# Kernel tuning notes

Measured on AMD Instinct MI355X. Metric: run time of the kernel, lower is better.

Reference implementation:

```python
import jax, jax.numpy as jnp
import numpy as np

TEMPERATURE = 0.1
NUM_CLASSES = 4  # matches fill_max of labels
NEG_INF = -1e9
EPS = 1e-6


def setup_inputs() -> dict:
    key = jax.random.key(0)
    k1, k2 = jax.random.split(key)
    emb = jax.random.normal(k1, (2, 128, 64, 64), dtype=jnp.float32)
    labels = jax.random.randint(k2, (2, 64, 64), 0, NUM_CLASSES, dtype=jnp.int32)
    return {"emb": emb, "labels": labels}


def reference(emb, labels):
    B, C, H, W = emb.shape
    e = emb.transpose(0, 2, 3, 1).reshape(B * H * W, C)      # [N, C]
    lab = labels.reshape(B * H * W)                           # [N]
    # F.normalize(dim=1) with eps clamp
    norm = jnp.maximum(jnp.linalg.norm(e, axis=1, keepdims=True), 1e-12)
    e = e / norm
    n = e.shape[0]
    logits = (e @ e.T) / TEMPERATURE                          # [N, N]
    diag = jnp.arange(n)
    logits = logits.at[diag, diag].set(NEG_INF)               # mask self
    ex = jnp.exp(logits)                                      # [N, N]
    same = lab[:, None] == lab[None, :]                       # [N, N] bool
    pos_sum = jnp.sum(jnp.where(same, ex, 0.0), axis=1)       # [N]
    tot_sum = jnp.sum(ex, axis=1)                             # [N]
    row_loss = -jnp.log(pos_sum / (tot_sum + EPS))            # [N]
    # per-class mean, averaged over classes present (== torch.unique loop)
    sums = jax.ops.segment_sum(row_loss, lab, num_segments=NUM_CLASSES)
    counts = jax.ops.segment_sum(jnp.ones_like(row_loss), lab, num_segments=NUM_CLASSES)
    present = counts > 0
    per_cls = jnp.where(present, sums / jnp.maximum(counts, 1.0), 0.0)
    return per_cls.sum() / present.sum()
```

## Files before the change

### kernel.cpp

```cpp
#include <hip/hip_runtime.h>
#include <hip/hip_bf16.h>

#define N_PIX 8192
#define C_DIM 128
#define HW 4096
#define PRESCALE 3.7982825f
#define NUM_CLASSES 4

typedef __attribute__((ext_vector_type(8))) short short8;
typedef __attribute__((ext_vector_type(4))) float float4v;


__global__ __launch_bounds__(256) void normscale_kernel(const float* __restrict__ emb,
                                                        unsigned short* __restrict__ ebfT,
                                                        float* __restrict__ pz) {
    const int tid = threadIdx.x;
    const int p16 = tid & 15;
    const int g = tid >> 4;
    const int n = blockIdx.x * 16 + p16;
    const int b = n >> 12;
    const int hw = n & (HW - 1);
    const float* base = emb + b * (C_DIM * HW) + hw;

    float v[8];
    float ss = 0.f;
#pragma unroll
    for (int i = 0; i < 8; ++i) {
        v[i] = base[(g * 8 + i) * HW];
        ss += v[i] * v[i];
    }
    ss += __shfl_xor(ss, 16, 64);
    ss += __shfl_xor(ss, 32, 64);
    __shared__ float red[4][16];
    const int wv = tid >> 6;
    if ((tid & 63) < 16) red[wv][p16] = ss;
    __syncthreads();
    float tot = red[0][p16] + red[1][p16] + red[2][p16] + red[3][p16];
    float inv = PRESCALE / fmaxf(sqrtf(tot), 1e-12f);

    unsigned short us[8];
#pragma unroll
    for (int i = 0; i < 8; ++i) {
        __hip_bfloat16 h = __float2bfloat16(v[i] * inv);
        us[i] = *reinterpret_cast<unsigned short*>(&h);
    }
    const int s = g >> 2, quad = g & 3;
    unsigned short* dst = ebfT + (((blockIdx.x * 4 + s) * 64 + quad * 16 + p16) << 3);
    *reinterpret_cast<short8*>(dst) = *reinterpret_cast<short8*>(us);

    if (blockIdx.x < 64) pz[blockIdx.x * 256 + tid] = 0.f;
}

__global__ __launch_bounds__(256, 4) void pairwise_kernel(const unsigned short* __restrict__ ebfT,
                                                          const int* __restrict__ lab,
                                                          float* __restrict__ pos,
                                                          float* __restrict__ tot) {
    const int bi = blockIdx.x;
    const int d = blockIdx.y + 1;
    if (d == 32 && bi >= 32) return;
    const int jp = (bi + d) & 63;
    const int Ipanel = bi << 7;
    const int Jpanel = jp << 7;

    const int wave = threadIdx.x >> 6;
    const int lane = threadIdx.x & 63;
    const int quad = lane >> 4;
    const int lq = lane & 15;

    const int I0 = Ipanel + wave * 32;

    __shared__ float2 cpart[4][8][64];

    short8 afrag[2][4];
#pragma unroll
    for (int a = 0; a < 2; ++a) {
        const unsigned short* ab = ebfT + ((((I0 >> 4) + a) * 4) * 64 + lane) * 8;
#pragma unroll
        for (int s = 0; s < 4; ++s)
            afrag[a][s] = *reinterpret_cast<const short8*>(ab + s * 512);
    }
    int lab_row[2][4];
#pragma unroll
    for (int a = 0; a < 2; ++a)
#pragma unroll
        for (int r = 0; r < 4; ++r) lab_row[a][r] = lab[I0 + a * 16 + quad * 4 + r];

    float tacc[2][4] = {};
    float pacc[2][4] = {};

    {
        const unsigned short* bbase = ebfT + ((Jpanel >> 4) * 4 * 64 + lane) * 8;
#pragma unroll 2
        for (int t = 0; t < 8; ++t) {
            const int lab_col = lab[Jpanel + t * 16 + lq];
            const unsigned short* bt = bbase + t * 2048;
            short8 bfrag[4];
#pragma unroll
            for (int s = 0; s < 4; ++s)
                bfrag[s] = *reinterpret_cast<const short8*>(bt + s * 512);

            float4v acc0 = {0.f, 0.f, 0.f, 0.f};
            float4v acc1 = {0.f, 0.f, 0.f, 0.f};
#pragma unroll
            for (int s = 0; s < 4; ++s) {
                acc0 = __builtin_amdgcn_mfma_f32_16x16x32_bf16(afrag[0][s], bfrag[s], acc0, 0, 0, 0);
                acc1 = __builtin_amdgcn_mfma_f32_16x16x32_bf16(afrag[1][s], bfrag[s], acc1, 0, 0, 0);
            }

            float colTs = 0.f, colPs = 0.f;
#pragma unroll
            for (int r = 0; r < 4; ++r) {
                float ex = __builtin_amdgcn_exp2f(acc0[r]);
                tacc[0][r] += ex;
                float pxe = (lab_row[0][r] == lab_col) ? ex : 0.f;
                pacc[0][r] += pxe;
                colTs += ex;
                colPs += pxe;
            }
#pragma unroll
            for (int r = 0; r < 4; ++r) {
                float ex = __builtin_amdgcn_exp2f(acc1[r]);
                tacc[1][r] += ex;
                float pxe = (lab_row[1][r] == lab_col) ? ex : 0.f;
                pacc[1][r] += pxe;
                colTs += ex;
                colPs += pxe;
            }
            cpart[wave][t][lane] = make_float2(colTs, colPs);
        }
    }

#define EPILOGUE(A, ACC, MASKED)                                            \
    {                                                                       \
        _Pragma("unroll") for (int r = 0; r < 4; ++r) {                     \
            float ex = __builtin_amdgcn_exp2f(ACC[r]);                      \
            if (MASKED) ex = (lq == quad * 4 + r) ? 0.f : ex;               \
            tacc[A][r] += ex;                                               \
            pacc[A][r] += (lab_row[A][r] == lab_col) ? ex : 0.f;            \
        }                                                                   \
    }
    if (d == 1) {
        const unsigned short* bbase = ebfT + ((Ipanel >> 4) * 4 * 64 + lane) * 8;
#pragma unroll 2
        for (int t = 0; t < 8; ++t) {
            const int J = Ipanel + t * 16;
            const int lab_col = lab[J + lq];
            const unsigned short* bt = bbase + t * 2048;
            short8 bfrag[4];
#pragma unroll
            for (int s = 0; s < 4; ++s)
                bfrag[s] = *reinterpret_cast<const short8*>(bt + s * 512);

            float4v acc0 = {0.f, 0.f, 0.f, 0.f};
            float4v acc1 = {0.f, 0.f, 0.f, 0.f};
#pragma unroll
            for (int s = 0; s < 4; ++s) {
                acc0 = __builtin_amdgcn_mfma_f32_16x16x32_bf16(afrag[0][s], bfrag[s], acc0, 0, 0, 0);
                acc1 = __builtin_amdgcn_mfma_f32_16x16x32_bf16(afrag[1][s], bfrag[s], acc1, 0, 0, 0);
            }
            if (J == I0) EPILOGUE(0, acc0, true) else EPILOGUE(0, acc0, false);
            if (J == I0 + 16) EPILOGUE(1, acc1, true) else EPILOGUE(1, acc1, false);
        }
    }
#undef EPILOGUE

#pragma unroll
    for (int a = 0; a < 2; ++a) {
#pragma unroll
        for (int r = 0; r < 4; ++r) {
            float t = tacc[a][r], p = pacc[a][r];
#pragma unroll
            for (int off = 1; off < 16; off <<= 1) {
                t += __shfl_xor(t, off, 64);
                p += __shfl_xor(p, off, 64);
            }
            if (lq == 0) {
                const int row = I0 + a * 16 + quad * 4 + r;
                atomicAdd(&tot[row], t);
                atomicAdd(&pos[row], p);
            }
        }
    }

    __syncthreads();
    if (threadIdx.x < 128) {
        const int j = threadIdx.x;
        const int tt = j >> 4, jl = j & 15;
        float st = 0.f, sp = 0.f;
#pragma unroll
        for (int w = 0; w < 4; ++w)
#pragma unroll
            for (int q = 0; q < 4; ++q) {
                float2 v = cpart[w][tt][q * 16 + jl];
                st += v.x;
                sp += v.y;
            }
        atomicAdd(&tot[Jpanel + j], st);
        atomicAdd(&pos[Jpanel + j], sp);
    }
}

__global__ __launch_bounds__(1024) void finalize_kernel(const float* __restrict__ pos,
                                                        const float* __restrict__ tot,
                                                        const int* __restrict__ lab,
                                                        float* __restrict__ out) {
    const int tid = threadIdx.x;
    float ls[NUM_CLASSES] = {0.f, 0.f, 0.f, 0.f};
    float lc[NUM_CLASSES] = {0.f, 0.f, 0.f, 0.f};
#pragma unroll
    for (int it = 0; it < N_PIX / 1024; ++it) {
        const int n = it * 1024 + tid;
        float rl = logf(tot[n] + 1e-6f) - logf(pos[n]);
        int c = lab[n];
#pragma unroll
        for (int k = 0; k < NUM_CLASSES; ++k) {
            if (c == k) {
                ls[k] += rl;
                lc[k] += 1.f;
            }
        }
    }
#pragma unroll
    for (int off = 1; off < 64; off <<= 1) {
#pragma unroll
        for (int k = 0; k < NUM_CLASSES; ++k) {
            ls[k] += __shfl_xor(ls[k], off, 64);
            lc[k] += __shfl_xor(lc[k], off, 64);
        }
    }
    __shared__ float ssum[16][NUM_CLASSES];
    __shared__ float scnt[16][NUM_CLASSES];
    const int wid = tid >> 6;
    if ((tid & 63) == 0) {
#pragma unroll
        for (int k = 0; k < NUM_CLASSES; ++k) {
            ssum[wid][k] = ls[k];
            scnt[wid][k] = lc[k];
        }
    }
    __syncthreads();
    if (tid == 0) {
        float acc = 0.f;
        int present = 0;
        for (int k = 0; k < NUM_CLASSES; ++k) {
            float s = 0.f, c = 0.f;
            for (int w = 0; w < 16; ++w) {
                s += ssum[w][k];
                c += scnt[w][k];
            }
            if (c > 0.f) {
                acc += s / c;
                present++;
            }
        }
        out[0] = acc / (float)(present > 0 ? present : 1);
    }
}

extern "C" void kernel_launch(void* const* d_in, const int* in_sizes, int n_in,
                              void* d_out, int out_size, void* d_ws, size_t ws_size,
                              hipStream_t stream) {
    const float* emb = (const float*)d_in[0];
    const int* lab = (const int*)d_in[1];
    float* out = (float*)d_out;

    unsigned short* ebfT = (unsigned short*)d_ws;
    float* pos = (float*)((char*)d_ws + N_PIX * C_DIM * 2);
    float* tot = pos + N_PIX;

    normscale_kernel<<<N_PIX / 16, 256, 0, stream>>>(emb, ebfT, pos);

    dim3 grid(64, 32);
    pairwise_kernel<<<grid, 256, 0, stream>>>(ebfT, lab, pos, tot);

    finalize_kernel<<<1, 1024, 0, stream>>>(pos, tot, lab, out);
}
```

Before: 87.78 us.

## Process two column panels per block and fuse finalize via last-block counter

Each pairwise block now handles two symmetric column panels instead of one, halving the grid to 64x16 and reusing the loaded A fragments across both panels. The separate finalize kernel is removed: a global atomic counter, zeroed in the normalize kernel, lets the last finishing block compute the per-class loss. This removes a kernel launch and the per-block overhead of loading A fragments, at the cost of a larger shared buffer, a threadfence and atomic per block, and a serial 256-thread finalize tail.

After: 144.1 us. 1.64x slower.

```diff
diff --git a/kernel.cpp b/kernel.cpp
--- a/kernel.cpp
+++ b/kernel.cpp
@@ -6,6 +6,7 @@
 #define HW 4096
 #define PRESCALE 3.7982825f
 #define NUM_CLASSES 4
+#define PAIR_BLOCKS (64 * 16)
 
 typedef __attribute__((ext_vector_type(8))) short short8;
 typedef __attribute__((ext_vector_type(4))) float float4v;
@@ -13,7 +14,8 @@
 
 __global__ __launch_bounds__(256) void normscale_kernel(const float* __restrict__ emb,
                                                         unsigned short* __restrict__ ebfT,
-                                                        float* __restrict__ pz) {
+                                                        float* __restrict__ pz,
+                                                        unsigned* __restrict__ cnt) {
     const int tid = threadIdx.x;
     const int p16 = tid & 15;
     const int g = tid >> 4;
@@ -49,27 +51,28 @@
     *reinterpret_cast<short8*>(dst) = *reinterpret_cast<short8*>(us);
 
     if (blockIdx.x < 64) pz[blockIdx.x * 256 + tid] = 0.f;
+    if (blockIdx.x == 64 && tid == 0) cnt[0] = 0u;
 }
 
 __global__ __launch_bounds__(256, 4) void pairwise_kernel(const unsigned short* __restrict__ ebfT,
                                                           const int* __restrict__ lab,
                                                           float* __restrict__ pos,
-                                                          float* __restrict__ tot) {
+                                                          float* __restrict__ tot,
+                                                          unsigned* __restrict__ cnt,
+                                                          float* __restrict__ out) {
     const int bi = blockIdx.x;
-    const int d = blockIdx.y + 1;
-    if (d == 32 && bi >= 32) return;
-    const int jp = (bi + d) & 63;
-    const int Ipanel = bi << 7;
-    const int Jpanel = jp << 7;
+    const int dd = blockIdx.y;
 
     const int wave = threadIdx.x >> 6;
     const int lane = threadIdx.x & 63;
     const int quad = lane >> 4;
     const int lq = lane & 15;
 
+    const int Ipanel = bi << 7;
     const int I0 = Ipanel + wave * 32;
-
-    __shared__ float2 cpart[4][8][64];
+    const bool has2 = !(dd == 15 && bi >= 32);
+
+    __shared__ float2 cpart[4][16][64];
 
     short8 afrag[2][4];
 #pragma unroll
@@ -88,7 +91,10 @@
     float tacc[2][4] = {};
     float pacc[2][4] = {};
 
-    {
+    for (int pp = 0; pp < 2; ++pp) {
+        if (pp == 1 && !has2) break;
+        const int jp = (bi + 2 * dd + 1 + pp) & 63;
+        const int Jpanel = jp << 7;
         const unsigned short* bbase = ebfT + ((Jpanel >> 4) * 4 * 64 + lane) * 8;
 #pragma unroll 2
         for (int t = 0; t < 8; ++t) {
@@ -126,7 +132,7 @@
                 colTs += ex;
                 colPs += pxe;
             }
-            cpart[wave][t][lane] = make_float2(colTs, colPs);
+            cpart[wave][pp * 8 + t][lane] = make_float2(colTs, colPs);
         }
     }
 
@@ -139,7 +145,7 @@
             pacc[A][r] += (lab_row[A][r] == lab_col) ? ex : 0.f;            \
         }                                                                   \
     }
-    if (d == 1) {
+    if (dd == 0) {
         const unsigned short* bbase = ebfT + ((Ipanel >> 4) * 4 * 64 + lane) * 8;
 #pragma unroll 2
         for (int t = 0; t < 8; ++t) {
@@ -183,77 +189,89 @@
     }
 
     __syncthreads();
-    if (threadIdx.x < 128) {
+    {
         const int j = threadIdx.x;
-        const int tt = j >> 4, jl = j & 15;
-        float st = 0.f, sp = 0.f;
-#pragma unroll
-        for (int w = 0; w < 4; ++w)
-#pragma unroll
-            for (int q = 0; q < 4; ++q) {
-                float2 v = cpart[w][tt][q * 16 + jl];
-                st += v.x;
-                sp += v.y;
-            }
-        atomicAdd(&tot[Jpanel + j], st);
-        atomicAdd(&pos[Jpanel + j], sp);
-    }
-}
-
-__global__ __launch_bounds__(1024) void finalize_kernel(const float* __restrict__ pos,
-                                                        const float* __restrict__ tot,
-                                                        const int* __restrict__ lab,
-                                                        float* __restrict__ out) {
-    const int tid = threadIdx.x;
-    float ls[NUM_CLASSES] = {0.f, 0.f, 0.f, 0.f};
-    float lc[NUM_CLASSES] = {0.f, 0.f, 0.f, 0.f};
-#pragma unroll
-    for (int it = 0; it < N_PIX / 1024; ++it) {
-        const int n = it * 1024 + tid;
-        float rl = logf(tot[n] + 1e-6f) - logf(pos[n]);
-        int c = lab[n];
-#pragma unroll
-        for (int k = 0; k < NUM_CLASSES; ++k) {
-            if (c == k) {
-                ls[k] += rl;
-                lc[k] += 1.f;
-            }
-        }
-    }
-#pragma unroll
-    for (int off = 1; off < 64; off <<= 1) {
-#pragma unroll
-        for (int k = 0; k < NUM_CLASSES; ++k) {
-            ls[k] += __shfl_xor(ls[k], off, 64);
-            lc[k] += __shfl_xor(lc[k], off, 64);
-        }
-    }
-    __shared__ float ssum[16][NUM_CLASSES];
-    __shared__ float scnt[16][NUM_CLASSES];
-    const int wid = tid >> 6;
-    if ((tid & 63) == 0) {
-#pragma unroll
-        for (int k = 0; k < NUM_CLASSES; ++k) {
-            ssum[wid][k] = ls[k];
-            scnt[wid][k] = lc[k];
-        }
-    }
-    __syncthreads();
-    if (tid == 0) {
-        float acc = 0.f;
-        int present = 0;
-        for (int k = 0; k < NUM_CLASSES; ++k) {
-            float s = 0.f, c = 0.f;
-            for (int w = 0; w < 16; ++w) {
-                s += ssum[w][k];
-                c += scnt[w][k];
-            }
-            if (c > 0.f) {
-                acc += s / c;
-                present++;
-            }
-        }
-        out[0] = acc / (float)(present > 0 ? present : 1);
+        const int pp = j >> 7;
+        if (pp == 0 || has2) {
+            const int jc = j & 127;
+            const int jp = (bi + 2 * dd + 1 + pp) & 63;
+            const int tt = pp * 8 + (jc >> 4);
+            const int jl = jc & 15;
+            float st = 0.f, sp = 0.f;
+#pragma unroll
+            for (int w = 0; w < 4; ++w)
+#pragma unroll
+                for (int q = 0; q < 4; ++q) {
+                    float2 v = cpart[w][tt][q * 16 + jl];
+                    st += v.x;
+                    sp += v.y;
+                }
+            atomicAdd(&tot[(jp << 7) + jc], st);
+            atomicAdd(&pos[(jp << 7) + jc], sp);
+        }
+    }
+
+    __threadfence();
+    __syncthreads();
+    __shared__ unsigned slast;
+    if (threadIdx.x == 0)
+        slast = (atomicAdd(cnt, 1u) == PAIR_BLOCKS - 1) ? 1u : 0u;
+    __syncthreads();
+    if (slast == 0u) return;
+
+    {
+        const int tid = threadIdx.x;
+        float ls[NUM_CLASSES] = {0.f, 0.f, 0.f, 0.f};
+        float lc[NUM_CLASSES] = {0.f, 0.f, 0.f, 0.f};
+#pragma unroll
+        for (int it = 0; it < N_PIX / 256; ++it) {
+            const int n = it * 256 + tid;
+            float tv = __hip_atomic_load(&tot[n], __ATOMIC_RELAXED, __HIP_MEMORY_SCOPE_AGENT);
+            float pv = __hip_atomic_load(&pos[n], __ATOMIC_RELAXED, __HIP_MEMORY_SCOPE_AGENT);
+            float rl = logf(tv + 1e-6f) - logf(pv);
+            int c = lab[n];
+#pragma unroll
+            for (int k = 0; k < NUM_CLASSES; ++k) {
+                if (c == k) {
+                    ls[k] += rl;
+                    lc[k] += 1.f;
+                }
+            }
+        }
+#pragma unroll
+        for (int off = 1; off < 64; off <<= 1) {
+#pragma unroll
+            for (int k = 0; k < NUM_CLASSES; ++k) {
+                ls[k] += __shfl_xor(ls[k], off, 64);
+                lc[k] += __shfl_xor(lc[k], off, 64);
+            }
+        }
+        __shared__ float fsum[4][NUM_CLASSES];
+        __shared__ float fcnt[4][NUM_CLASSES];
+        if ((tid & 63) == 0) {
+#pragma unroll
+            for (int k = 0; k < NUM_CLASSES; ++k) {
+                fsum[wave][k] = ls[k];
+                fcnt[wave][k] = lc[k];
+            }
+        }
+        __syncthreads();
+        if (tid == 0) {
+            float acc = 0.f;
+            int present = 0;
+            for (int k = 0; k < NUM_CLASSES; ++k) {
+                float s = 0.f, c = 0.f;
+                for (int w = 0; w < 4; ++w) {
+                    s += fsum[w][k];
+                    c += fcnt[w][k];
+                }
+                if (c > 0.f) {
+                    acc += s / c;
+                    present++;
+                }
+            }
+            out[0] = acc / (float)(present > 0 ? present : 1);
+        }
     }
 }
 
@@ -267,11 +285,10 @@
     unsigned short* ebfT = (unsigned short*)d_ws;
     float* pos = (float*)((char*)d_ws + N_PIX * C_DIM * 2);
     float* tot = pos + N_PIX;
-
-    normscale_kernel<<<N_PIX / 16, 256, 0, stream>>>(emb, ebfT, pos);
-
-    dim3 grid(64, 32);
-    pairwise_kernel<<<grid, 256, 0, stream>>>(ebfT, lab, pos, tot);
-
-    finalize_kernel<<<1, 1024, 0, stream>>>(pos, tot, lab, out);
+    unsigned* cnt = (unsigned*)(tot + N_PIX);
+
+    normscale_kernel<<<N_PIX / 16, 256, 0, stream>>>(emb, ebfT, pos, cnt);
+
+    dim3 grid(64, 16);
+    pairwise_kernel<<<grid, 256, 0, stream>>>(ebfT, lab, pos, tot, cnt, out);
 }
```
